# Optimization experiments

Hardware: AMD Instinct MI355X
Metric: run time of the kernel (lower is better)

The kernel has to match this reference:

```python
import jax, jax.numpy as jnp
import numpy as np

N_QUBIT = 22
N_LAYERS = 2
D_LOGICAL = 2  # num_logical_dim (one logical qubit)
DIM = 2 ** N_QUBIT


def _apply_ry(psi, th, q):
    # psi: (B, 2^n) complex64; Ry(th) on qubit q (q=0 is the most significant bit)
    half = th * 0.5
    c = jnp.cos(half).astype(jnp.complex64)
    s = jnp.sin(half).astype(jnp.complex64)
    psi4 = psi.reshape(psi.shape[0], 2 ** q, 2, -1)
    p0, p1 = psi4[:, :, 0], psi4[:, :, 1]
    out = jnp.stack([c * p0 - s * p1, s * p0 + c * p1], axis=2)
    return out.reshape(psi.shape)


def _apply_cnot(psi, c, t):
    a, b = (c, t) if c < t else (t, c)
    right = 2 ** (N_QUBIT - b - 1)
    mid = 2 ** (b - a - 1)
    psi6 = psi.reshape(psi.shape[0], 2 ** a, 2, mid, 2, right)
    if c < t:
        # control is axis 2; flip target axis 4 where control==1
        psi6 = psi6.at[:, :, 1, :, :, :].set(psi6[:, :, 1, :, ::-1, :])
    else:
        # control is axis 4; flip target axis 2 where control==1
        psi6 = psi6.at[:, :, :, :, 1, :].set(psi6[:, :, ::-1, :, 1, :])
    return psi6.reshape(psi.shape)


def _apply_pauli(psi, p, q):
    psi4 = psi.reshape(psi.shape[0], 2 ** q, 2, -1)
    p0, p1 = psi4[:, :, 0], psi4[:, :, 1]
    if p == 'X':
        out = jnp.stack([p1, p0], axis=2)
    elif p == 'Y':
        out = jnp.stack([-1j * p1, 1j * p0], axis=2)
    else:  # Z
        out = jnp.stack([p0, -p1], axis=2)
    return out.reshape(psi.shape)


def _encode(theta):
    # q0[i, i] = 1 for the logical basis states, then run the circuit
    psi = jnp.zeros((D_LOGICAL, DIM), jnp.complex64)
    psi = psi.at[jnp.arange(D_LOGICAL), jnp.arange(D_LOGICAL)].set(1.0)
    for l in range(N_LAYERS):
        for q in range(N_QUBIT):
            psi = _apply_ry(psi, theta[l, q], q)
        for q in range(N_QUBIT):
            psi = _apply_cnot(psi, q, (q + 1) % N_QUBIT)
    return psi


def _kl_loss(theta):
    psi = _encode(theta)  # (D_LOGICAL, 2^n)
    # Knill-Laflamme inner products T_e[i,j] = <psi_i| E_e |psi_j> for all weight-1 Paulis
    Ts = []
    for q in range(N_QUBIT):
        for p in ('X', 'Y', 'Z'):
            epsi = _apply_pauli(psi, p, q)
            Ts.append(jnp.einsum('is,js->ij', psi.conj(), epsi))
    T = jnp.stack(Ts)  # (3*N_QUBIT, D_LOGICAL, D_LOGICAL)
    diag = jnp.diagonal(T, axis1=1, axis2=2)
    lam = diag.mean(axis=1)  # per-error lambda_e
    res = T - lam[:, None, None] * jnp.eye(D_LOGICAL, dtype=T.dtype)
    # loss_type == 'L2'
    return jnp.sum(jnp.abs(res) ** 2)


def setup_inputs() -> dict:
    key = jax.random.key(0)
    theta = jax.random.normal(key, (N_LAYERS, N_QUBIT), dtype=jnp.float32)
    return {"theta": theta}


def reference(theta):
    return _kl_loss(theta)
```

## Files before the change

### kernel.cpp

```cpp
#include <hip/hip_runtime.h>

#define NQ 22
#define DIMN (1u << NQ)

struct MaskSet {
    unsigned L[NQ];
    unsigned Linv[NQ];
    unsigned xm[NQ];
    unsigned zm[NQ];
    unsigned frowHi[5];
};

constexpr MaskSet buildMasks() {
    MaskSet M{};
    for (int b = 0; b < NQ; ++b) M.L[b] = 1u << b;
    for (int q = 0; q < NQ; ++q) {
        int bc = NQ - 1 - q, bt = NQ - 1 - ((q + 1) % NQ);
        M.L[bt] ^= M.L[bc];
    }
    unsigned mat[NQ] = {}, aug[NQ] = {};
    for (int b = 0; b < NQ; ++b) { mat[b] = M.L[b]; aug[b] = 1u << b; }
    for (int col = 0; col < NQ; ++col) {
        int piv = col;
        while (!((mat[piv] >> col) & 1u)) ++piv;
        unsigned tm = mat[piv]; mat[piv] = mat[col]; mat[col] = tm;
        unsigned ta = aug[piv]; aug[piv] = aug[col]; aug[col] = ta;
        for (int r = 0; r < NQ; ++r)
            if (r != col && ((mat[r] >> col) & 1u)) { mat[r] ^= mat[col]; aug[r] ^= aug[col]; }
    }
    for (int b = 0; b < NQ; ++b) M.Linv[b] = aug[b];
    for (int j = 0; j < NQ; ++j) {
        int b = NQ - 1 - j;
        unsigned xmv = 0;
        for (int r = 0; r < NQ; ++r)
            if ((aug[r] >> b) & 1u) xmv |= 1u << r;
        M.xm[j] = xmv;
        M.zm[j] = M.L[b];
    }
    for (int j = 0; j < 5; ++j) {
        unsigned f = 0;
        for (int r = 0; r < NQ; ++r)
            if ((aug[r] >> (17 + j)) & 1u) f |= 1u << r;
        M.frowHi[j] = f;
    }
    return M;
}
constexpr int topbit_c(unsigned v) { int b = 0; while (v >> (b + 1)) ++b; return b; }
constexpr unsigned unionHi() {
    MaskSet M = buildMasks();
    unsigned u = 0;
    for (int j = 0; j < 5; ++j) u |= M.frowHi[j];
    return u;
}
static_assert((unionHi() & 0xFFFFu) == 0, "frowHi must only touch bits 16..21");

__device__ __forceinline__ float wave_sum(float v) {
    v += __shfl_down(v, 32); v += __shfl_down(v, 16); v += __shfl_down(v, 8);
    v += __shfl_down(v, 4);  v += __shfl_down(v, 2);  v += __shfl_down(v, 1);
    return v;
}
__device__ __forceinline__ float fflip(float v, unsigned sbit31) {
    return __int_as_float(__float_as_int(v) ^ (int)sbit31);
}
__device__ __forceinline__ unsigned ph4(unsigned g) { return g ^ ((g >> 6) & 3u); }

__global__ __launch_bounds__(256) void k_prep(const float* __restrict__ theta,
                                              float* __restrict__ acc,
                                              float* __restrict__ trig) {
    int t = threadIdx.x;
    acc[t] = 0.f;
    if (t < 2 * NQ) {
        int l = t / NQ, q = t % NQ, b = NQ - 1 - q;
        float h = 0.5f * theta[t];
        trig[l * 2 * NQ + b]      = cosf(h);
        trig[l * 2 * NQ + NQ + b] = sinf(h);
    }
}

__global__ __launch_bounds__(256, 1) void k_genHi(float* __restrict__ phi,
                                                  const float* __restrict__ trig,
                                                  float* __restrict__ acc) {
    constexpr MaskSet M = buildMasks();
    __shared__ float red[4 * 12];
    unsigned base = blockIdx.x * 256u + threadIdx.x;
    unsigned P0 = 0;
#pragma unroll
    for (int b = 0; b < NQ; ++b)
        P0 |= ((unsigned)__popc(base & M.Linv[b]) & 1u) << b;
    float pc = 1.f;
#pragma unroll
    for (int b = 1; b < 16; ++b) {
        float cvb = trig[b], svb = trig[NQ + b];
        pc *= ((P0 >> b) & 1u) ? svb : cvb;
    }
    float cv0 = trig[0], sv0 = trig[NQ];
    float C0 = pc * ((P0 & 1u) ? sv0 : cv0);
    float C1 = pc * ((P0 & 1u) ? cv0 : -sv0);
    float cb[6], sb[6];
#pragma unroll
    for (int k = 0; k < 6; ++k) { cb[k] = trig[16 + k]; sb[k] = trig[NQ + 16 + k]; }
    unsigned u0 = P0 >> 16;
    float v0[32], v1[32];
#pragma unroll
    for (int e = 0; e < 32; ++e) {
        unsigned F = 0;
        if (e & 1)  F ^= M.frowHi[0];
        if (e & 2)  F ^= M.frowHi[1];
        if (e & 4)  F ^= M.frowHi[2];
        if (e & 8)  F ^= M.frowHi[3];
        if (e & 16) F ^= M.frowHi[4];
        unsigned u = u0 ^ (F >> 16);
        float vp = (u & 1u) ? sb[0] : cb[0];
#pragma unroll
        for (int k = 1; k < 6; ++k) vp *= ((u >> k) & 1u) ? sb[k] : cb[k];
        v0[e] = vp * C0;
        v1[e] = vp * C1;
    }
    float c2[5], s2[5];
#pragma unroll
    for (int j = 0; j < 5; ++j) {
        c2[j] = trig[2 * NQ + 17 + j];
        s2[j] = trig[3 * NQ + 17 + j];
    }
#pragma unroll
    for (int j = 0; j < 5; ++j) {
#pragma unroll
        for (int e = 0; e < 32; ++e) {
            if (!(e & (1 << j))) {
                int e1 = e | (1 << j);
                float a0 = v0[e], a1 = v0[e1];
                v0[e]  = c2[j] * a0 - s2[j] * a1;
                v0[e1] = s2[j] * a0 + c2[j] * a1;
                float b0 = v1[e], b1 = v1[e1];
                v1[e]  = c2[j] * b0 - s2[j] * b1;
                v1[e1] = s2[j] * b0 + c2[j] * b1;
            }
        }
    }
#pragma unroll
    for (int e = 0; e < 32; ++e) {
        unsigned a = base | ((unsigned)e << 17);
        phi[a] = v0[e];
        phi[DIMN + a] = v1[e];
    }
    int lane = threadIdx.x & 63, w = threadIdx.x >> 6;
#pragma unroll
    for (int i = 1; i <= 3; ++i) {
        unsigned ex  = M.xm[i] >> 17;
        unsigned zme = M.zm[i] >> 17;
        float t00 = 0.f, t11 = 0.f, t01 = 0.f, u01 = 0.f;
#pragma unroll
        for (int e = 0; e < 32; ++e) {
            int ep = e ^ (int)ex;
            t00 += v0[e] * v0[ep];
            t11 += v1[e] * v1[ep];
            float p = v0[e] * v1[ep];
            t01 += p;
            unsigned sg = ((unsigned)__popc((unsigned)ep & zme) & 1u) << 31;
            u01 += fflip(p, sg);
        }
        float vals[4] = { t00, t11, t01, u01 };
#pragma unroll
        for (int j = 0; j < 4; ++j) {
            float v = wave_sum(vals[j]);
            if (lane == 0) red[w * 12 + (i - 1) * 4 + j] = v;
        }
    }
    __syncthreads();
    int t = threadIdx.x;
    if (t < 12) {
        float r = red[t] + red[12 + t] + red[24 + t] + red[36 + t];
        atomicAdd(&acc[4 + t], r);
    }
}

__global__ __launch_bounds__(256, 1) void k_mid(float* __restrict__ phi,
                                                const float* __restrict__ trig,
                                                float* __restrict__ acc) {
    constexpr MaskSet M = buildMasks();
    __shared__ float red[4 * 20];
    unsigned tid = blockIdx.x * 256u + threadIdx.x;
    unsigned base = (tid & 0xFFFu) | ((tid >> 12) << 18);
    float v0[64], v1[64];
#pragma unroll
    for (int e = 0; e < 64; ++e) {
        unsigned a = base | ((unsigned)e << 12);
        v0[e] = phi[a];
        v1[e] = phi[DIMN + a];
    }
    float c[5], s[5];
#pragma unroll
    for (int j = 0; j < 5; ++j) {
        c[j] = trig[2 * NQ + 12 + j];
        s[j] = trig[3 * NQ + 12 + j];
    }
#pragma unroll
    for (int j = 0; j < 5; ++j) {
#pragma unroll
        for (int e = 0; e < 64; ++e) {
            if (!(e & (1 << j))) {
                int e1 = e | (1 << j);
                float a0 = v0[e], a1 = v0[e1];
                v0[e]  = c[j] * a0 - s[j] * a1;
                v0[e1] = s[j] * a0 + c[j] * a1;
                float b0 = v1[e], b1 = v1[e1];
                v1[e]  = c[j] * b0 - s[j] * b1;
                v1[e1] = s[j] * b0 + c[j] * b1;
            }
        }
    }
#pragma unroll
    for (int e = 0; e < 64; ++e) {
        unsigned a = base | ((unsigned)e << 12);
        phi[a] = v0[e];
        phi[DIMN + a] = v1[e];
    }
    int lane = threadIdx.x & 63, w = threadIdx.x >> 6;
#pragma unroll
    for (int i = 4; i <= 8; ++i) {
        unsigned ex  = M.xm[i] >> 12;
        unsigned zme = (M.zm[i] >> 12) & 63u;
        unsigned bs31 = ((unsigned)__popc(base & M.zm[i]) & 1u) << 31;
        float t00 = 0.f, t11 = 0.f, t01 = 0.f, u01 = 0.f;
#pragma unroll
        for (int e = 0; e < 64; ++e) {
            int ep = e ^ (int)ex;
            t00 += v0[e] * v0[ep];
            t11 += v1[e] * v1[ep];
            float p = v0[e] * v1[ep];
            t01 += p;
            unsigned sg = ((unsigned)__popc((unsigned)ep & zme) & 1u) << 31;
            u01 += fflip(p, sg ^ bs31);
        }
        float vals[4] = { t00, t11, t01, u01 };
#pragma unroll
        for (int j = 0; j < 4; ++j) {
            float v = wave_sum(vals[j]);
            if (lane == 0) red[w * 20 + (i - 4) * 4 + j] = v;
        }
    }
    __syncthreads();
    int t = threadIdx.x;
    if (t < 20) {
        float r = red[t] + red[20 + t] + red[40 + t] + red[60 + t];
        atomicAdd(&acc[16 + t], r);
    }
}

__global__ __launch_bounds__(256) void k_low(float* __restrict__ phi,
                                             const float* __restrict__ trig,
                                             float* __restrict__ acc) {
    constexpr MaskSet M = buildMasks();
    __shared__ float As[4096];
    __shared__ float Bs[4096];
    __shared__ float red[4 * 44];
    float4* As4 = (float4*)As;
    float4* Bs4 = (float4*)Bs;
    int t = threadIdx.x;
    unsigned base = blockIdx.x * 4096u;
    float a[16], b[16];

    {
        const float4* g0 = (const float4*)(phi + base);
        const float4* g1 = (const float4*)(phi + DIMN + base);
#pragma unroll
        for (int k = 0; k < 4; ++k) {
            float4 va = g0[4 * t + k];
            a[4 * k] = va.x; a[4 * k + 1] = va.y; a[4 * k + 2] = va.z; a[4 * k + 3] = va.w;
            float4 vb = g1[4 * t + k];
            b[4 * k] = vb.x; b[4 * k + 1] = vb.y; b[4 * k + 2] = vb.z; b[4 * k + 3] = vb.w;
        }
#pragma unroll
        for (int g = 0; g < 4; ++g) {
            float c = trig[2 * NQ + g], s = trig[3 * NQ + g];
#pragma unroll
            for (int e = 0; e < 16; ++e) {
                if (!(e & (1 << g))) {
                    int e1 = e | (1 << g);
                    float x0 = a[e], x1 = a[e1];
                    a[e] = c * x0 - s * x1; a[e1] = s * x0 + c * x1;
                    float y0 = b[e], y1 = b[e1];
                    b[e] = c * y0 - s * y1; b[e1] = s * y0 + c * y1;
                }
            }
        }
        unsigned sw = (unsigned)(t >> 4) & 3u;
#pragma unroll
        for (int k = 0; k < 4; ++k) {
            unsigned f = ((unsigned)(4 * t + k)) ^ sw;
            As4[f] = make_float4(a[4 * k], a[4 * k + 1], a[4 * k + 2], a[4 * k + 3]);
            Bs4[f] = make_float4(b[4 * k], b[4 * k + 1], b[4 * k + 2], b[4 * k + 3]);
        }
    }
    __syncthreads();

    {
        unsigned lo = (unsigned)t & 15u, hi = (unsigned)t >> 4;
        unsigned swz = (hi & 3u) << 2;
#pragma unroll
        for (int j = 0; j < 16; ++j) {
            unsigned i = lo | ((unsigned)j << 4) | (hi << 8);
            a[j] = As[i ^ swz];
            b[j] = Bs[i ^ swz];
        }
#pragma unroll
        for (int g = 0; g < 4; ++g) {
            float c = trig[2 * NQ + 4 + g], s = trig[3 * NQ + 4 + g];
#pragma unroll
            for (int e = 0; e < 16; ++e) {
                if (!(e & (1 << g))) {
                    int e1 = e | (1 << g);
                    float x0 = a[e], x1 = a[e1];
                    a[e] = c * x0 - s * x1; a[e1] = s * x0 + c * x1;
                    float y0 = b[e], y1 = b[e1];
                    b[e] = c * y0 - s * y1; b[e1] = s * y0 + c * y1;
                }
            }
        }
#pragma unroll
        for (int j = 0; j < 16; ++j) {
            unsigned i = lo | ((unsigned)j << 4) | (hi << 8);
            As[i ^ swz] = a[j];
            Bs[i ^ swz] = b[j];
        }
    }
    __syncthreads();

    {
#pragma unroll
        for (int j = 0; j < 16; ++j) {
            unsigned i = (unsigned)t | ((unsigned)j << 8);
            unsigned p = i ^ (((unsigned)j & 3u) << 2);
            a[j] = As[p];
            b[j] = Bs[p];
        }
#pragma unroll
        for (int g = 0; g < 4; ++g) {
            float c = trig[2 * NQ + 8 + g], s = trig[3 * NQ + 8 + g];
#pragma unroll
            for (int e = 0; e < 16; ++e) {
                if (!(e & (1 << g))) {
                    int e1 = e | (1 << g);
                    float x0 = a[e], x1 = a[e1];
                    a[e] = c * x0 - s * x1; a[e1] = s * x0 + c * x1;
                    float y0 = b[e], y1 = b[e1];
                    b[e] = c * y0 - s * y1; b[e1] = s * y0 + c * y1;
                }
            }
        }
#pragma unroll
        for (int j = 0; j < 16; ++j) {
            unsigned i = (unsigned)t | ((unsigned)j << 8);
            phi[base + i] = a[j];
            phi[DIMN + base + i] = b[j];
            unsigned p = i ^ (((unsigned)j & 3u) << 2);
            As[p] = a[j];
            Bs[p] = b[j];
        }
    }

    float SSv[3], z0v[3], z1v[3], z2v[3], d4v[3];
    {
#pragma unroll
        for (int c = 0; c < 3; ++c) {
            float p[16];
#pragma unroll
            for (int j = 0; j < 16; ++j)
                p[j] = (c == 0) ? a[j] * a[j] : (c == 1) ? b[j] * b[j] : a[j] * b[j];
            float s1[8], d1[8];
#pragma unroll
            for (int j = 0; j < 8; ++j) { s1[j] = p[j] + p[j + 8]; d1[j] = p[j] - p[j + 8]; }
            float s2[4], d2[4];
#pragma unroll
            for (int j = 0; j < 4; ++j) { s2[j] = s1[j] + s1[j + 4]; d2[j] = d1[j] - d1[j + 4]; }
            float d3a = d2[0] - d2[2], d3b = d2[1] - d2[3];
            SSv[c] = (s2[0] + s2[1]) + (s2[2] + s2[3]);
            z0v[c] = ((d1[0] + d1[1]) + (d1[2] + d1[3])) + ((d1[4] + d1[5]) + (d1[6] + d1[7]));
            z1v[c] = (d2[0] + d2[1]) + (d2[2] + d2[3]);
            z2v[c] = d3a + d3b;
            d4v[c] = d3a - d3b;
        }
    }
    {
        unsigned Wt = (unsigned)t;
        Wt ^= Wt >> 1; Wt ^= Wt >> 2; Wt ^= Wt >> 4;
        int lane = t & 63, w = t >> 6;
#pragma unroll
        for (int c = 0; c < 3; ++c) {
            float v;
            v = wave_sum(SSv[c]); if (lane == 0) red[w * 39 + c] = v;
            v = wave_sum(z0v[c]); if (lane == 0) red[w * 39 + 3 + c] = v;
            v = wave_sum(z1v[c]); if (lane == 0) red[w * 39 + 6 + c] = v;
            v = wave_sum(z2v[c]); if (lane == 0) red[w * 39 + 9 + c] = v;
            v = wave_sum(d4v[c]); if (lane == 0) red[w * 39 + 12 + c] = v;
#pragma unroll
            for (int k = 4; k < 12; ++k) {
                unsigned sb = ((Wt >> (11 - k)) & 1u) << 31;
                v = wave_sum(fflip(d4v[c], sb));
                if (lane == 0) red[w * 39 + 3 + 3 * k + c] = v;
            }
        }
    }
    __syncthreads();
    if (t < 66) {
        int c = t % 3, q = t / 3;
        int slot = (q == 0 || q == 21) ? (3 + 33 + c) : (q < 10 ? c : 3 + 3 * (q - 10) + c);
        float val = red[slot] + red[39 + slot] + red[78 + slot] + red[117 + slot];
        unsigned sg = (unsigned)__popc(base & M.zm[q]) & 1u;
        atomicAdd(&acc[4 * NQ + 3 * q + c], sg ? -val : val);
    }
    __syncthreads();

    int lane = t & 63, w = t >> 6;
#pragma unroll
    for (int i = 0; i < 11; ++i) {
        unsigned m = M.xm[10 + i], zm = M.zm[10 + i];
        unsigned zb = (unsigned)__popc(base & zm) & 1u;
        float t00 = 0.f, t11 = 0.f, t01 = 0.f, u01 = 0.f;
        if (i < 10) {
            int gb = topbit_c(M.xm[10 + i]) - 2;
            unsigned mg4 = m >> 2;
            unsigned swap2 = m & 3u;
#pragma unroll
            for (int r = 0; r < 2; ++r) {
                unsigned gc = (unsigned)t + 256u * r;
                unsigned g = ((gc >> gb) << (gb + 1)) | (gc & ((1u << gb) - 1u));
                unsigned gx = g ^ mg4;
                float4 a0 = As4[ph4(g)],  a1 = Bs4[ph4(g)];
                float4 b0 = As4[ph4(gx)], b1 = Bs4[ph4(gx)];
                if (swap2) {
                    b0 = make_float4(b0.z, b0.w, b0.x, b0.y);
                    b1 = make_float4(b1.z, b1.w, b1.x, b1.y);
                }
                unsigned szg = ((unsigned)__popc((g << 2) & zm) + zb) & 1u;
                unsigned szx = ((unsigned)__popc((gx << 2) & zm) + zb) & 1u;
                unsigned fg = szg << 31, fx = szx << 31;
                const float* A0 = &a0.x; const float* A1 = &a1.x;
                const float* B0 = &b0.x; const float* B1 = &b1.x;
#pragma unroll
                for (int j = 0; j < 4; ++j) {
                    t00 += A0[j] * B0[j];
                    t11 += A1[j] * B1[j];
                    float p = A0[j] * B1[j], r2 = B0[j] * A1[j];
                    t01 += p + r2;
                    u01 += fflip(p, fx) + fflip(r2, fg);
                }
            }
            t00 *= 2.f; t11 *= 2.f;
        } else {
#pragma unroll
            for (int k = 0; k < 4; ++k) {
                unsigned g = (unsigned)t + 256u * k;
                float4 a0 = As4[ph4(g)], a1 = Bs4[ph4(g)];
                unsigned szg = ((unsigned)__popc((g << 2) & zm) + zb) & 1u;
                const float* A0 = &a0.x; const float* A1 = &a1.x;
#pragma unroll
                for (int j = 0; j < 4; ++j) {
                    int jx = j ^ 3;
                    float p = A0[j] * A0[jx];
                    float q2 = A1[j] * A1[jx];
                    float cr = A0[j] * A1[jx];
                    t00 += p; t11 += q2; t01 += cr;
                    unsigned sj = ((unsigned)(jx >> 1) & 1u) ^ szg;
                    u01 += fflip(cr, sj << 31);
                }
            }
        }
        float vals[4] = { t00, t11, t01, u01 };
#pragma unroll
        for (int j = 0; j < 4; ++j) {
            float v = wave_sum(vals[j]);
            if (lane == 0) red[w * 44 + 4 * i + j] = v;
        }
    }
    __syncthreads();
    if (t < 44) {
        float r = red[t] + red[44 + t] + red[88 + t] + red[132 + t];
        atomicAdd(&acc[40 + t], r);
    }
}

struct Meas3Arg { unsigned xm[3]; unsigned zm[3]; int gbit[3]; int qn[3]; };

__global__ __launch_bounds__(256) void k_measS(const float* __restrict__ phi,
                                               float* __restrict__ acc,
                                               Meas3Arg M) {
    __shared__ float red[16];
    int t = threadIdx.x;
    int slice = blockIdx.y;
    unsigned m = M.xm[slice], zm = M.zm[slice];
    int gb = M.gbit[slice];
    unsigned mg4 = m >> 2;
    unsigned ml2 = m & 3u;
    unsigned zl = zm & 3u;
    unsigned pg31[4], px31[4];
#pragma unroll
    for (int j = 0; j < 4; ++j) {
        pg31[j] = (((unsigned)__popc((unsigned)j & zl) & 1u) << 31);
        px31[j] = (((unsigned)__popc(((unsigned)j ^ ml2) & zl) & 1u) << 31);
    }
    unsigned tid = blockIdx.x * 256u + (unsigned)t;
    const float4* p0 = (const float4*)phi;
    const float4* p1 = (const float4*)(phi + DIMN);
    float t00 = 0.f, t11 = 0.f, t01 = 0.f, u01 = 0.f;
#pragma unroll
    for (int it = 0; it < 8; ++it) {
        unsigned gc = tid + (unsigned)it * 65536u;
        unsigned g = ((gc >> gb) << (gb + 1)) | (gc & ((1u << gb) - 1u));
        unsigned gx = g ^ mg4;
        float4 a0 = p0[g], a1 = p1[g];
        float4 b0 = p0[gx], b1 = p1[gx];
        if (ml2) {
            b0 = make_float4(b0.y, b0.x, b0.w, b0.z);
            b1 = make_float4(b1.y, b1.x, b1.w, b1.z);
        }
        unsigned fg = (((unsigned)__popc((g << 2) & zm) & 1u) << 31);
        unsigned fx = (((unsigned)__popc((gx << 2) & zm) & 1u) << 31);
        const float* A0 = &a0.x; const float* A1 = &a1.x;
        const float* B0 = &b0.x; const float* B1 = &b1.x;
#pragma unroll
        for (int j = 0; j < 4; ++j) {
            t00 += A0[j] * B0[j];
            t11 += A1[j] * B1[j];
            float p = A0[j] * B1[j], r = B0[j] * A1[j];
            t01 += p + r;
            u01 += fflip(p, fx ^ px31[j]) + fflip(r, fg ^ pg31[j]);
        }
    }
    t00 *= 2.f; t11 *= 2.f;
    int lane = t & 63, w = t >> 6;
    float vals[4] = { t00, t11, t01, u01 };
#pragma unroll
    for (int j = 0; j < 4; ++j) {
        float v = wave_sum(vals[j]);
        if (lane == 0) red[w * 4 + j] = v;
    }
    __syncthreads();
    if (t < 4) {
        float r = red[t] + red[4 + t] + red[8 + t] + red[12 + t];
        atomicAdd(&acc[4 * M.qn[slice] + t], r);
    }
}

__global__ __launch_bounds__(64) void k_final(const float* __restrict__ acc,
                                              float* __restrict__ out) {
    int t = threadIdx.x;
    float v = 0.f;
    if (t < NQ) {
        float t00 = acc[4 * t], t11 = acc[4 * t + 1];
        float t01 = acc[4 * t + 2], u01 = acc[4 * t + 3];
        float d = t00 - t11;
        v = 0.5f * d * d + 2.f * t01 * t01 + 2.f * u01 * u01;
    } else if (t < 2 * NQ) {
        int q = t - NQ;
        float z0 = acc[4 * NQ + 3 * q], z1 = acc[4 * NQ + 3 * q + 1];
        float zz = acc[4 * NQ + 3 * q + 2];
        float d = z0 - z1;
        v = 0.5f * d * d + 2.f * zz * zz;
    }
    v += __shfl_down(v, 32); v += __shfl_down(v, 16); v += __shfl_down(v, 8);
    v += __shfl_down(v, 4);  v += __shfl_down(v, 2);  v += __shfl_down(v, 1);
    if (t == 0) out[0] = v;
}

extern "C" void kernel_launch(void* const* d_in, const int* in_sizes, int n_in,
                              void* d_out, int out_size, void* d_ws, size_t ws_size,
                              hipStream_t stream) {
    const float* theta = (const float*)d_in[0];
    float* out  = (float*)d_out;
    float* ws   = (float*)d_ws;
    float* phi  = ws;
    float* acc  = ws + 2 * (size_t)DIMN;
    float* trig = acc + 256;

    constexpr MaskSet M = buildMasks();

    Meas3Arg m3;
    const int qs[3] = { 0, 9, 21 };
    for (int i = 0; i < 3; ++i) {
        int q = qs[i];
        m3.xm[i] = M.xm[q]; m3.zm[i] = M.zm[q];
        m3.gbit[i] = topbit_c(M.xm[q]) - 2;
        m3.qn[i] = q;
    }

    k_prep<<<1, 256, 0, stream>>>(theta, acc, trig);
    k_genHi<<<512, 256, 0, stream>>>(phi, trig, acc);
    k_mid<<<256, 256, 0, stream>>>(phi, trig, acc);
    k_low<<<1024, 256, 0, stream>>>(phi, trig, acc);
    k_measS<<<dim3(256, 3), 256, 0, stream>>>(phi, acc, m3);
    k_final<<<1, 64, 0, stream>>>(acc, out);
}
```

Baseline: 166.5 us.

## Halve k_mid per-thread state, move qubit-4 term to measS, register-path k_low

The mid-range rotation kernel now keeps 32 amplitudes per thread instead of 64 and launches twice as many blocks. The aim is to cut register pressure and raise parallelism in a kernel that was bounded to one block per CU. Because a thread no longer spans the bit that qubit 4's error operator flips, that Knill-Laflamme term moves into k_measS as a fourth slice, which adds another full read of the state vector. In k_low, the terms for qubits 10 to 12 are now computed directly from the per-thread registers instead of from shared memory.

```diff
diff --git a/kernel.cpp b/kernel.cpp
--- a/kernel.cpp
+++ b/kernel.cpp
@@ -174,16 +174,16 @@
     }
 }
 
-__global__ __launch_bounds__(256, 1) void k_mid(float* __restrict__ phi,
-                                                const float* __restrict__ trig,
-                                                float* __restrict__ acc) {
+__global__ __launch_bounds__(256, 1) void k_midA(float* __restrict__ phi,
+                                                 const float* __restrict__ trig,
+                                                 float* __restrict__ acc) {
     constexpr MaskSet M = buildMasks();
-    __shared__ float red[4 * 20];
+    __shared__ float red[4 * 16];
     unsigned tid = blockIdx.x * 256u + threadIdx.x;
-    unsigned base = (tid & 0xFFFu) | ((tid >> 12) << 18);
-    float v0[64], v1[64];
-#pragma unroll
-    for (int e = 0; e < 64; ++e) {
+    unsigned base = (tid & 0xFFFu) | ((tid >> 12) << 17);
+    float v0[32], v1[32];
+#pragma unroll
+    for (int e = 0; e < 32; ++e) {
         unsigned a = base | ((unsigned)e << 12);
         v0[e] = phi[a];
         v1[e] = phi[DIMN + a];
@@ -197,7 +197,7 @@
 #pragma unroll
     for (int j = 0; j < 5; ++j) {
 #pragma unroll
-        for (int e = 0; e < 64; ++e) {
+        for (int e = 0; e < 32; ++e) {
             if (!(e & (1 << j))) {
                 int e1 = e | (1 << j);
                 float a0 = v0[e], a1 = v0[e1];
@@ -210,20 +210,20 @@
         }
     }
 #pragma unroll
-    for (int e = 0; e < 64; ++e) {
+    for (int e = 0; e < 32; ++e) {
         unsigned a = base | ((unsigned)e << 12);
         phi[a] = v0[e];
         phi[DIMN + a] = v1[e];
     }
     int lane = threadIdx.x & 63, w = threadIdx.x >> 6;
 #pragma unroll
-    for (int i = 4; i <= 8; ++i) {
-        unsigned ex  = M.xm[i] >> 12;
-        unsigned zme = (M.zm[i] >> 12) & 63u;
+    for (int i = 5; i <= 8; ++i) {
+        unsigned ex  = (M.xm[i] >> 12) & 31u;
+        unsigned zme = (M.zm[i] >> 12) & 31u;
         unsigned bs31 = ((unsigned)__popc(base & M.zm[i]) & 1u) << 31;
         float t00 = 0.f, t11 = 0.f, t01 = 0.f, u01 = 0.f;
 #pragma unroll
-        for (int e = 0; e < 64; ++e) {
+        for (int e = 0; e < 32; ++e) {
             int ep = e ^ (int)ex;
             t00 += v0[e] * v0[ep];
             t11 += v1[e] * v1[ep];
@@ -236,14 +236,14 @@
 #pragma unroll
         for (int j = 0; j < 4; ++j) {
             float v = wave_sum(vals[j]);
-            if (lane == 0) red[w * 20 + (i - 4) * 4 + j] = v;
+            if (lane == 0) red[w * 16 + (i - 5) * 4 + j] = v;
         }
     }
     __syncthreads();
     int t = threadIdx.x;
-    if (t < 20) {
-        float r = red[t] + red[20 + t] + red[40 + t] + red[60 + t];
-        atomicAdd(&acc[16 + t], r);
+    if (t < 16) {
+        float r = red[t] + red[16 + t] + red[32 + t] + red[48 + t];
+        atomicAdd(&acc[20 + t], r);
     }
 }
 
@@ -412,8 +412,34 @@
     __syncthreads();
 
     int lane = t & 63, w = t >> 6;
-#pragma unroll
-    for (int i = 0; i < 11; ++i) {
+
+#pragma unroll
+    for (int i = 0; i < 3; ++i) {
+        constexpr int qn0 = 10;
+        unsigned je  = (M.xm[qn0 + i] >> 8) & 15u;
+        unsigned zmj = (M.zm[qn0 + i] >> 8) & 15u;
+        unsigned zb31 = ((unsigned)__popc(base & M.zm[qn0 + i]) & 1u) << 31;
+        float t00 = 0.f, t11 = 0.f, t01 = 0.f, u01 = 0.f;
+#pragma unroll
+        for (int j = 0; j < 16; ++j) {
+            int jp = j ^ (int)je;
+            t00 += a[j] * a[jp];
+            t11 += b[j] * b[jp];
+            float p = a[j] * b[jp];
+            t01 += p;
+            unsigned sg = ((unsigned)__popc((unsigned)jp & zmj) & 1u) << 31;
+            u01 += fflip(p, sg ^ zb31);
+        }
+        float vals[4] = { t00, t11, t01, u01 };
+#pragma unroll
+        for (int j = 0; j < 4; ++j) {
+            float v = wave_sum(vals[j]);
+            if (lane == 0) red[w * 44 + 4 * i + j] = v;
+        }
+    }
+
+#pragma unroll
+    for (int i = 3; i < 11; ++i) {
         unsigned m = M.xm[10 + i], zm = M.zm[10 + i];
         unsigned zb = (unsigned)__popc(base & zm) & 1u;
         float t00 = 0.f, t11 = 0.f, t01 = 0.f, u01 = 0.f;
@@ -480,11 +506,11 @@
     }
 }
 
-struct Meas3Arg { unsigned xm[3]; unsigned zm[3]; int gbit[3]; int qn[3]; };
+struct Meas4Arg { unsigned xm[4]; unsigned zm[4]; int gbit[4]; int qn[4]; };
 
 __global__ __launch_bounds__(256) void k_measS(const float* __restrict__ phi,
                                                float* __restrict__ acc,
-                                               Meas3Arg M) {
+                                               Meas4Arg M) {
     __shared__ float red[16];
     int t = threadIdx.x;
     int slice = blockIdx.y;
@@ -575,19 +601,19 @@
 
     constexpr MaskSet M = buildMasks();
 
-    Meas3Arg m3;
-    const int qs[3] = { 0, 9, 21 };
-    for (int i = 0; i < 3; ++i) {
+    Meas4Arg m4;
+    const int qs[4] = { 0, 4, 9, 21 };
+    for (int i = 0; i < 4; ++i) {
         int q = qs[i];
-        m3.xm[i] = M.xm[q]; m3.zm[i] = M.zm[q];
-        m3.gbit[i] = topbit_c(M.xm[q]) - 2;
-        m3.qn[i] = q;
+        m4.xm[i] = M.xm[q]; m4.zm[i] = M.zm[q];
+        m4.gbit[i] = topbit_c(M.xm[q]) - 2;
+        m4.qn[i] = q;
     }
 
     k_prep<<<1, 256, 0, stream>>>(theta, acc, trig);
     k_genHi<<<512, 256, 0, stream>>>(phi, trig, acc);
-    k_mid<<<256, 256, 0, stream>>>(phi, trig, acc);
+    k_midA<<<512, 256, 0, stream>>>(phi, trig, acc);
     k_low<<<1024, 256, 0, stream>>>(phi, trig, acc);
-    k_measS<<<dim3(256, 3), 256, 0, stream>>>(phi, acc, m3);
+    k_measS<<<dim3(256, 4), 256, 0, stream>>>(phi, acc, m4);
     k_final<<<1, 64, 0, stream>>>(acc, out);
 }
```

After: 165.0 us. Within noise of the previous version (-0.9%).
